# Kernel optimization log

Measured on AMD Instinct MI355X. Metric: run time of the kernel, lower is better.

## Reference

```python
import jax, jax.numpy as jnp
import numpy as np

B, D = 32768, 512
ANCHOR_CLASS = 0  # module starts with self.a = 0; labels guarantee >1 sample of class 0


def setup_inputs() -> dict:
    key = jax.random.key(0)
    k0, k1, k2, k3, k4 = jax.random.split(key, 5)
    return {
        "label": jax.random.randint(k0, (B,), 0, 7, dtype=jnp.int64),
        "p_t": jax.random.normal(k1, (B, D), dtype=jnp.float32),
        "p_a": jax.random.normal(k2, (B, D), dtype=jnp.float32),
        "s_t": jax.random.normal(k3, (B, D), dtype=jnp.float32),
        "s_a": jax.random.normal(k4, (B, D), dtype=jnp.float32),
    }


def _modality_loss(X, anchor_idx, pos_mask, neg_mask):
    # cosine similarity of every row vs. the anchor row, fully vectorized
    anchor = X[anchor_idx]                                 # [D]
    dots = X @ anchor                                      # [B]
    cos = dots / (jnp.linalg.norm(X, axis=1) * jnp.linalg.norm(anchor))
    pos_cnt = jnp.sum(pos_mask)
    neg_cnt = jnp.sum(neg_mask)
    pos_score = jnp.where(pos_cnt > 0,
                          jnp.sum(jnp.where(pos_mask, cos, 0.0)) / jnp.maximum(pos_cnt, 1),
                          0.0)
    neg_score = jnp.where(neg_cnt > 0,
                          jnp.sum(jnp.where(neg_mask, cos, 0.0)) / jnp.maximum(neg_cnt, 1),
                          0.0)
    return 2.0 - pos_score + neg_score


def reference(label, p_t, p_a, s_t, s_a):
    a = ANCHOR_CLASS
    is_class = (label == a)
    # deterministic anchor: first sample of the anchor class (original draws one
    # uniformly; any member gives the same math structure)
    anchor_idx = jnp.argmax(is_class)
    not_anchor = jnp.arange(label.shape[0]) != anchor_idx
    pos_mask = is_class & not_anchor
    neg_mask = (~is_class) & not_anchor

    losses = jnp.stack([
        _modality_loss(p_t, anchor_idx, pos_mask, neg_mask),
        _modality_loss(p_a, anchor_idx, pos_mask, neg_mask),
        _modality_loss(s_t, anchor_idx, pos_mask, neg_mask),
        _modality_loss(s_a, anchor_idx, pos_mask, neg_mask),
    ])
    return jnp.mean(losses)
```

## Files before the change

### kernel.cpp

```cpp
#include <hip/hip_runtime.h>

#define B_ROWS   32768
#define D_DIM    512
#define NBLOCKS  1024
#define TPB      256
#define NWAVES   (NBLOCKS * (TPB / 64))
#define RPW      (B_ROWS / NWAVES)

struct Ws {
    unsigned anchor_idx;
    int      cnt0;
};

__device__ __forceinline__ float dot4(float4 a, float4 b) {
    return a.x * b.x + a.y * b.y + a.z * b.z + a.w * b.w;
}

__device__ __forceinline__ float fold_reduce8(const float v[8], int lane) {
    float w[4];
    #pragma unroll
    for (int i = 0; i < 4; ++i) {
        float send = (lane & 32) ? v[i] : v[i + 4];
        float rcv  = __shfl_xor(send, 32);
        w[i] = ((lane & 32) ? v[i + 4] : v[i]) + rcv;
    }
    float u[2];
    #pragma unroll
    for (int i = 0; i < 2; ++i) {
        float send = (lane & 16) ? w[i] : w[i + 2];
        float rcv  = __shfl_xor(send, 16);
        u[i] = ((lane & 16) ? w[i + 2] : w[i]) + rcv;
    }
    float t;
    {
        float send = (lane & 8) ? u[0] : u[1];
        float rcv  = __shfl_xor(send, 8);
        t = ((lane & 8) ? u[1] : u[0]) + rcv;
    }
    t += __shfl_xor(t, 4);
    t += __shfl_xor(t, 2);
    t += __shfl_xor(t, 1);
    return t;
}

__device__ __forceinline__ void loadrow(float4 x[8], const float* const X[4],
                                        unsigned r, int lane) {
    #pragma unroll
    for (int m = 0; m < 4; ++m) {
        const float4* Xr = (const float4*)(X[m] + (size_t)r * D_DIM) + lane * 2;
        x[2 * m]     = Xr[0];
        x[2 * m + 1] = Xr[1];
    }
}

__device__ __forceinline__ void process_row(const float4 x[8], const float4 an[8],
                                            int lane, int lab, unsigned r,
                                            unsigned aidx, float inv_mine,
                                            float& posAcc, float& negAcc) {
    float v[8];
    #pragma unroll
    for (int m = 0; m < 4; ++m) {
        v[m]     = dot4(x[2 * m], an[2 * m]) + dot4(x[2 * m + 1], an[2 * m + 1]);
        v[m + 4] = dot4(x[2 * m], x[2 * m]) + dot4(x[2 * m + 1], x[2 * m + 1]);
    }
    float t     = fold_reduce8(v, lane);
    float other = __shfl_xor(t, 32);
    if (((lane & 39) == 0) && (r != aidx)) {
        float c = t * rsqrtf(other) * inv_mine;
        if (lab == 0) posAcc += c; else negAcc += c;
    }
}

__global__ void scan_labels_kernel(const int* __restrict__ label, Ws* ws) {
    int tid = blockIdx.x * blockDim.x + threadIdx.x;
    int stride = gridDim.x * blockDim.x;
    int cnt = 0;
    unsigned mymin = 0xFFFFFFFFu;
    for (int i = tid; i < B_ROWS; i += stride) {
        if (label[i] == 0) {
            cnt++;
            mymin = mymin < (unsigned)i ? mymin : (unsigned)i;
        }
    }
    for (int off = 32; off; off >>= 1) {
        cnt += __shfl_xor(cnt, off);
        unsigned o = (unsigned)__shfl_xor((int)mymin, off);
        mymin = mymin < o ? mymin : o;
    }
    if ((threadIdx.x & 63) == 0) {
        if (cnt) atomicAdd(&ws->cnt0, cnt);
        if (mymin != 0xFFFFFFFFu) atomicMin(&ws->anchor_idx, mymin);
    }
}

__launch_bounds__(TPB, 2)
__global__ void cos_accum_kernel(const int* __restrict__ label,
                                 const float* __restrict__ p_t,
                                 const float* __restrict__ p_a,
                                 const float* __restrict__ s_t,
                                 const float* __restrict__ s_a,
                                 const Ws* __restrict__ ws,
                                 float* __restrict__ partials) {
    const float* X[4] = {p_t, p_a, s_t, s_a};
    __shared__ float red[TPB / 64][8];

    const unsigned aidx = ws->anchor_idx;
    const int lane = threadIdx.x & 63;
    const int wid  = threadIdx.x >> 6;
    const int gwave = blockIdx.x * (TPB / 64) + wid;

    float4 an[8];
    #pragma unroll
    for (int m = 0; m < 4; ++m) {
        const float4* A = (const float4*)(X[m] + (size_t)aidx * D_DIM) + lane * 2;
        an[2 * m]     = A[0];
        an[2 * m + 1] = A[1];
    }

    float va[8];
    #pragma unroll
    for (int m = 0; m < 4; ++m) {
        va[m]     = dot4(an[2 * m], an[2 * m]) + dot4(an[2 * m + 1], an[2 * m + 1]);
        va[m + 4] = 0.f;
    }
    float inv_mine = rsqrtf(fold_reduce8(va, lane));

    float posAcc = 0.f, negAcc = 0.f;

    unsigned rA = (unsigned)gwave;
    int labA = label[rA];
    float4 xa[8];
    loadrow(xa, X, rA, lane);

    #pragma unroll
    for (int k = 0; k < RPW; k += 2) {
        unsigned rB = rA + NWAVES;
        int labB = label[rB];
        float4 xb[8];
        loadrow(xb, X, rB, lane);

        process_row(xa, an, lane, labA, rA, aidx, inv_mine, posAcc, negAcc);

        unsigned rA2 = rA + 2 * NWAVES;
        if (k + 2 < RPW) {
            labA = label[rA2];
            loadrow(xa, X, rA2, lane);
        }

        process_row(xb, an, lane, labB, rB, aidx, inv_mine, posAcc, negAcc);
        rA = rA2;
    }

    if ((lane & 39) == 0) {
        int m = lane >> 3;
        red[wid][m]     = posAcc;
        red[wid][4 + m] = negAcc;
    }
    __syncthreads();
    if (threadIdx.x < 8) {
        int j = threadIdx.x;
        partials[blockIdx.x * 8 + j] = red[0][j] + red[1][j] + red[2][j] + red[3][j];
    }
}

__global__ void finalize_kernel(const Ws* __restrict__ ws,
                                const float* __restrict__ partials,
                                float* __restrict__ out) {
    __shared__ float red[256];
    int t = threadIdx.x;
    int j = t & 7;
    float s = 0.f;
    for (int r = t >> 3; r < NBLOCKS; r += 32)
        s += partials[r * 8 + j];
    red[t] = s;
    __syncthreads();
    if (t < 8) {
        float tot = 0.f;
        #pragma unroll
        for (int k = 0; k < 32; ++k) tot += red[k * 8 + t];
        red[t] = tot;
    }
    __syncthreads();
    if (t == 0) {
        int cnt0 = ws->cnt0;
        float pos_cnt = (float)(cnt0 - 1);
        float neg_cnt = (float)(B_ROWS - cnt0);
        float total = 0.f;
        #pragma unroll
        for (int m = 0; m < 4; ++m) {
            float ps = (pos_cnt > 0.f) ? red[m]     / fmaxf(pos_cnt, 1.f) : 0.f;
            float ns = (neg_cnt > 0.f) ? red[4 + m] / fmaxf(neg_cnt, 1.f) : 0.f;
            total += 2.0f - ps + ns;
        }
        out[0] = total * 0.25f;
    }
}

extern "C" void kernel_launch(void* const* d_in, const int* in_sizes, int n_in,
                              void* d_out, int out_size, void* d_ws, size_t ws_size,
                              hipStream_t stream) {
    const int*   label = (const int*)  d_in[0];
    const float* p_t   = (const float*)d_in[1];
    const float* p_a   = (const float*)d_in[2];
    const float* s_t   = (const float*)d_in[3];
    const float* s_a   = (const float*)d_in[4];
    Ws* ws = (Ws*)d_ws;
    float* partials = (float*)d_ws + 64;

    hipMemsetAsync(d_ws, 0xFF, sizeof(unsigned), stream);
    hipMemsetAsync((char*)d_ws + sizeof(unsigned), 0, sizeof(int), stream);

    scan_labels_kernel <<<64,      256, 0, stream>>>(label, ws);
    cos_accum_kernel   <<<NBLOCKS, TPB, 0, stream>>>(label, p_t, p_a, s_t, s_a, ws, partials);
    finalize_kernel    <<<1,       256, 0, stream>>>(ws, partials, (float*)d_out);
}
```

Measured before the change: 67.88 us.

## Stage anchor rows in LDS, double grid, vectorize label scan, merge memsets

The four anchor rows are now staged in shared memory instead of being held in registers. The main loop drops its manual double-buffered prefetch for a simple unrolled loop, and the grid doubles to 2048 blocks with the occupancy hint removed. The label scan reads int4 vectors in a single pass over 32 blocks, and the two workspace memsets become one 0xFF memset, so the count starts at -1 and finalize adjusts for that. The aim is to cut register pressure, raise occupancy and reduce launch overhead on this memory-bound pass, at the cost of LDS reads on every row and the loss of explicit load/compute overlap.

```diff
diff --git a/kernel.cpp b/kernel.cpp
--- a/kernel.cpp
+++ b/kernel.cpp
@@ -2,7 +2,7 @@
 
 #define B_ROWS   32768
 #define D_DIM    512
-#define NBLOCKS  1024
+#define NBLOCKS  2048
 #define TPB      256
 #define NWAVES   (NBLOCKS * (TPB / 64))
 #define RPW      (B_ROWS / NWAVES)
@@ -43,45 +43,17 @@
     return t;
 }
 
-__device__ __forceinline__ void loadrow(float4 x[8], const float* const X[4],
-                                        unsigned r, int lane) {
-    #pragma unroll
-    for (int m = 0; m < 4; ++m) {
-        const float4* Xr = (const float4*)(X[m] + (size_t)r * D_DIM) + lane * 2;
-        x[2 * m]     = Xr[0];
-        x[2 * m + 1] = Xr[1];
-    }
-}
-
-__device__ __forceinline__ void process_row(const float4 x[8], const float4 an[8],
-                                            int lane, int lab, unsigned r,
-                                            unsigned aidx, float inv_mine,
-                                            float& posAcc, float& negAcc) {
-    float v[8];
-    #pragma unroll
-    for (int m = 0; m < 4; ++m) {
-        v[m]     = dot4(x[2 * m], an[2 * m]) + dot4(x[2 * m + 1], an[2 * m + 1]);
-        v[m + 4] = dot4(x[2 * m], x[2 * m]) + dot4(x[2 * m + 1], x[2 * m + 1]);
-    }
-    float t     = fold_reduce8(v, lane);
-    float other = __shfl_xor(t, 32);
-    if (((lane & 39) == 0) && (r != aidx)) {
-        float c = t * rsqrtf(other) * inv_mine;
-        if (lab == 0) posAcc += c; else negAcc += c;
-    }
-}
-
 __global__ void scan_labels_kernel(const int* __restrict__ label, Ws* ws) {
     int tid = blockIdx.x * blockDim.x + threadIdx.x;
-    int stride = gridDim.x * blockDim.x;
-    int cnt = 0;
+    const int4* L4 = (const int4*)label;
+    int4 v = L4[tid];
+    int cnt = (v.x == 0) + (v.y == 0) + (v.z == 0) + (v.w == 0);
+    unsigned base = (unsigned)tid * 4;
     unsigned mymin = 0xFFFFFFFFu;
-    for (int i = tid; i < B_ROWS; i += stride) {
-        if (label[i] == 0) {
-            cnt++;
-            mymin = mymin < (unsigned)i ? mymin : (unsigned)i;
-        }
-    }
+    if (v.w == 0) mymin = base + 3;
+    if (v.z == 0) mymin = base + 2;
+    if (v.y == 0) mymin = base + 1;
+    if (v.x == 0) mymin = base;
     for (int off = 32; off; off >>= 1) {
         cnt += __shfl_xor(cnt, off);
         unsigned o = (unsigned)__shfl_xor((int)mymin, off);
@@ -93,7 +65,7 @@
     }
 }
 
-__launch_bounds__(TPB, 2)
+__launch_bounds__(TPB)
 __global__ void cos_accum_kernel(const int* __restrict__ label,
                                  const float* __restrict__ p_t,
                                  const float* __restrict__ p_a,
@@ -102,53 +74,63 @@
                                  const Ws* __restrict__ ws,
                                  float* __restrict__ partials) {
     const float* X[4] = {p_t, p_a, s_t, s_a};
-    __shared__ float red[TPB / 64][8];
+    __shared__ float4 anc[4][D_DIM / 4];
+    __shared__ float  red[TPB / 64][8];
 
     const unsigned aidx = ws->anchor_idx;
     const int lane = threadIdx.x & 63;
     const int wid  = threadIdx.x >> 6;
     const int gwave = blockIdx.x * (TPB / 64) + wid;
 
-    float4 an[8];
-    #pragma unroll
-    for (int m = 0; m < 4; ++m) {
-        const float4* A = (const float4*)(X[m] + (size_t)aidx * D_DIM) + lane * 2;
-        an[2 * m]     = A[0];
-        an[2 * m + 1] = A[1];
+    for (int idx = threadIdx.x; idx < 4 * (D_DIM / 4); idx += TPB) {
+        int m = idx >> 7;
+        int j = idx & 127;
+        anc[m][j] = ((const float4*)(X[m] + (size_t)aidx * D_DIM))[j];
     }
+    __syncthreads();
 
-    float va[8];
-    #pragma unroll
-    for (int m = 0; m < 4; ++m) {
-        va[m]     = dot4(an[2 * m], an[2 * m]) + dot4(an[2 * m + 1], an[2 * m + 1]);
-        va[m + 4] = 0.f;
+    float inv_mine;
+    {
+        float va[8];
+        #pragma unroll
+        for (int m = 0; m < 4; ++m) {
+            float4 a0 = anc[m][lane * 2];
+            float4 a1 = anc[m][lane * 2 + 1];
+            va[m]     = dot4(a0, a0) + dot4(a1, a1);
+            va[m + 4] = 0.f;
+        }
+        inv_mine = rsqrtf(fold_reduce8(va, lane));
     }
-    float inv_mine = rsqrtf(fold_reduce8(va, lane));
 
     float posAcc = 0.f, negAcc = 0.f;
 
-    unsigned rA = (unsigned)gwave;
-    int labA = label[rA];
-    float4 xa[8];
-    loadrow(xa, X, rA, lane);
+    #pragma unroll
+    for (int k = 0; k < RPW; ++k) {
+        unsigned r = (unsigned)gwave + (unsigned)k * NWAVES;
+        int lab = label[r];
 
-    #pragma unroll
-    for (int k = 0; k < RPW; k += 2) {
-        unsigned rB = rA + NWAVES;
-        int labB = label[rB];
-        float4 xb[8];
-        loadrow(xb, X, rB, lane);
-
-        process_row(xa, an, lane, labA, rA, aidx, inv_mine, posAcc, negAcc);
-
-        unsigned rA2 = rA + 2 * NWAVES;
-        if (k + 2 < RPW) {
-            labA = label[rA2];
-            loadrow(xa, X, rA2, lane);
+        float4 x[8];
+        #pragma unroll
+        for (int m = 0; m < 4; ++m) {
+            const float4* Xr = (const float4*)(X[m] + (size_t)r * D_DIM) + lane * 2;
+            x[2 * m]     = Xr[0];
+            x[2 * m + 1] = Xr[1];
         }
 
-        process_row(xb, an, lane, labB, rB, aidx, inv_mine, posAcc, negAcc);
-        rA = rA2;
+        float v[8];
+        #pragma unroll
+        for (int m = 0; m < 4; ++m) {
+            float4 b0 = anc[m][lane * 2];
+            float4 b1 = anc[m][lane * 2 + 1];
+            v[m]     = dot4(x[2 * m], b0)       + dot4(x[2 * m + 1], b1);
+            v[m + 4] = dot4(x[2 * m], x[2 * m]) + dot4(x[2 * m + 1], x[2 * m + 1]);
+        }
+        float t     = fold_reduce8(v, lane);
+        float other = __shfl_xor(t, 32);
+        if (((lane & 39) == 0) && (r != aidx)) {
+            float c = t * rsqrtf(other) * inv_mine;
+            if (lab == 0) posAcc += c; else negAcc += c;
+        }
     }
 
     if ((lane & 39) == 0) {
@@ -182,9 +164,8 @@
     }
     __syncthreads();
     if (t == 0) {
-        int cnt0 = ws->cnt0;
-        float pos_cnt = (float)(cnt0 - 1);
-        float neg_cnt = (float)(B_ROWS - cnt0);
+        float pos_cnt = (float)ws->cnt0;
+        float neg_cnt = (float)(B_ROWS - (ws->cnt0 + 1));
         float total = 0.f;
         #pragma unroll
         for (int m = 0; m < 4; ++m) {
@@ -207,10 +188,9 @@
     Ws* ws = (Ws*)d_ws;
     float* partials = (float*)d_ws + 64;
 
-    hipMemsetAsync(d_ws, 0xFF, sizeof(unsigned), stream);
-    hipMemsetAsync((char*)d_ws + sizeof(unsigned), 0, sizeof(int), stream);
+    hipMemsetAsync(d_ws, 0xFF, 8, stream);
 
-    scan_labels_kernel <<<64,      256, 0, stream>>>(label, ws);
+    scan_labels_kernel <<<32,      TPB, 0, stream>>>(label, ws);
     cos_accum_kernel   <<<NBLOCKS, TPB, 0, stream>>>(label, p_t, p_a, s_t, s_a, ws, partials);
-    finalize_kernel    <<<1,       256, 0, stream>>>(ws, partials, (float*)d_out);
+    finalize_kernel    <<<1,       TPB, 0, stream>>>(ws, partials, (float*)d_out);
 }
```

Result: slower. 71.38 us (+5.2%).
